# Optimization experiments

Measured on AMD Instinct MI355X. Metric: run time of the kernel, lower is better.

The kernel has to match this reference:

```python
import jax, jax.numpy as jnp
import numpy as np

B, K, D, DICT, C = 2048, 32, 768, 24576, 64


def setup_inputs() -> dict:
    key = jax.random.key(0)
    ks = jax.random.split(key, 9)
    up_vals = jax.random.uniform(ks[0], (B, K), dtype=jnp.float32)
    up_decoder_w = jax.random.normal(ks[1], (D, DICT), dtype=jnp.float32) * 0.02
    down_encoder_w = jax.random.normal(ks[2], (DICT, D), dtype=jnp.float32) * 0.02
    up_encoder_w = jax.random.normal(ks[3], (DICT, D), dtype=jnp.float32) * 0.02
    b_dec = jax.random.normal(ks[4], (D,), dtype=jnp.float32) * 0.02
    up_indices = jax.random.randint(ks[5], (B, K), 0, DICT)
    down_indices = jax.random.randint(ks[6], (B, K), 0, DICT)
    conn = jax.random.randint(ks[7], (DICT, C), 0, DICT)
    drop = jax.random.uniform(ks[8], (DICT, C)) < 0.1
    connections = jnp.where(drop, -1, conn)
    return {
        "up_vals": up_vals,
        "up_decoder_w": up_decoder_w,
        "down_encoder_w": down_encoder_w,
        "up_encoder_w": up_encoder_w,
        "b_dec": b_dec,
        "up_indices": up_indices,
        "down_indices": down_indices,
        "connections": connections,
    }


def reference(up_vals, up_decoder_w, down_encoder_w, up_encoder_w, b_dec,
              up_indices, down_indices, connections):
    # allowed upstream features per active downstream feature: [B, k_down, C]
    allowed = connections[down_indices]
    valid = allowed != -1
    # match[b,i,c,j] = allowed[b,i,c] == up_indices[b,j] (and slot valid)
    match = (allowed[..., None] == up_indices[:, None, None, :]) & valid[..., None]
    # multiplicity of each (down i, up j) pair across the C slots: [B, k_down, k_up]
    mult = match.sum(axis=2).astype(up_vals.dtype)
    # gather active decoder/encoder vectors
    act_up = up_decoder_w.T[up_indices]          # [B, k_up, D]
    act_down = down_encoder_w[down_indices]      # [B, k_down, D]
    # virtual weights between active down and up features
    vw = jnp.einsum('bid,bjd->bij', act_down, act_up)  # [B, k_down, k_up]
    contributions = jnp.einsum('bij,bij->bi', vw, mult * up_vals[:, None, :])
    # bias contribution (note: indexed by up_indices, broadcast add as in source)
    b_dec_contrib = up_encoder_w @ b_dec         # [DICT]
    return contributions + b_dec_contrib[up_indices]
```

## Files before the change

kernel.cpp:

```cpp
#include <hip/hip_runtime.h>

#define B_    2048
#define K_    32
#define D_    768
#define DICT_ 24576
#define C_    64

#define PAIR_CAP (1 << 18)
#define CCHUNK   512
#define DCHUNK   16
#define NCC      (DICT_ / CCHUNK)
#define NDC      (D_ / DCHUNK)

#define BDC_F (PAIR_CAP * 4)
#define CNT_F (BDC_F + DICT_)
#define T_F   (CNT_F + 1)
#define WS_FLOATS (T_F + PAIR_CAP)

__global__ void bdc_kernel(const float* __restrict__ up_enc,
                           const float* __restrict__ b_dec,
                           float* __restrict__ bdc,
                           int* __restrict__ cnt) {
    if (blockIdx.x == 0 && threadIdx.x == 0) cnt[0] = 0;
    int wave = threadIdx.x >> 6;
    int lane = threadIdx.x & 63;
    int row  = blockIdx.x * 4 + wave;
    const float4* rp = (const float4*)(up_enc + (size_t)row * D_);
    const float4* bp = (const float4*)b_dec;
    float acc = 0.f;
    #pragma unroll
    for (int i = 0; i < 3; ++i) {
        float4 a = rp[lane + 64 * i];
        float4 b = bp[lane + 64 * i];
        acc += a.x * b.x + a.y * b.y + a.z * b.z + a.w * b.w;
    }
    #pragma unroll
    for (int off = 32; off; off >>= 1) acc += __shfl_xor(acc, off);
    if (lane == 0) bdc[row] = acc;
}

__global__ void scan_kernel(const float* __restrict__ up_vals,
                            const float* __restrict__ bdc,
                            const int*   __restrict__ up_idx,
                            const int*   __restrict__ down_idx,
                            const int*   __restrict__ conn,
                            int*  __restrict__ cnt,
                            int*  __restrict__ tArr,
                            int4* __restrict__ recArr,
                            float* __restrict__ out) {
    int wave = threadIdx.x >> 6;
    int lane = threadIdx.x & 63;
    int item = blockIdx.x * 4 + wave;
    int b    = item >> 5;

    int di = down_idx[item];
    int allowed = conn[(size_t)di * C_ + lane];
    bool valid = allowed >= 0;
    int   myup  = up_idx[b * K_ + (lane & 31)];
    float myval = up_vals[b * K_ + (lane & 31)];

    if (lane == 0) out[item] = bdc[up_idx[item]];

    unsigned jm = 0u;
    #pragma unroll
    for (int j = 0; j < K_; ++j) {
        int tgt = __builtin_amdgcn_readlane(myup, j);
        jm |= (valid && (allowed == tgt)) ? (1u << j) : 0u;
    }

    if (__ballot(jm != 0u)) {
        #pragma unroll 1
        for (int j = 0; j < K_; ++j) {
            unsigned long long m = __ballot((jm >> j) & 1u);
            if (m != 0) {
                int   t = __shfl(myup, j);
                float w = (float)__popcll(m) * __shfl(myval, j);
                if (lane == 0) {
                    int pos = atomicAdd(cnt, 1);
                    if (pos < PAIR_CAP) {
                        tArr[pos]   = t;
                        recArr[pos] = make_int4(item, di, __float_as_int(w), 0);
                    }
                }
            }
        }
    }
}

__global__ __launch_bounds__(256) void pair_dot_kernel(const float* __restrict__ A,
                                                       const float* __restrict__ down_enc,
                                                       const int*  __restrict__ cnt,
                                                       const int*  __restrict__ tArr,
                                                       const int4* __restrict__ recArr,
                                                       float* __restrict__ out) {
    __shared__ float tile[DCHUNK * CCHUNK];
    __shared__ int   lidx[512];
    __shared__ int   lcnt;
    int tid = threadIdx.x;
    if (tid == 0) lcnt = 0;
    __syncthreads();

    int cc = blockIdx.x, dc = blockIdx.y;
    int c0 = cc * CCHUNK, d0 = dc * DCHUNK;

    int n = *cnt; if (n > PAIR_CAP) n = PAIR_CAP;
    for (int i = tid; i < n; i += 256) {
        if ((tArr[i] >> 9) == cc) {
            int s = atomicAdd(&lcnt, 1);
            if (s < 512) lidx[s] = i;
        }
    }
    __syncthreads();
    int ln = lcnt < 512 ? lcnt : 512;
    if (ln == 0) return;

    #pragma unroll
    for (int k = 0; k < 8; ++k) {
        int l  = tid + 256 * k;
        int r  = l >> 7, fi = l & 127;
        ((float4*)tile)[l] = *(const float4*)(A + (size_t)(d0 + r) * DICT_ + c0 + 4 * fi);
    }
    __syncthreads();

    for (int i = tid; i < ln; i += 256) {
        int idx = lidx[i];
        int4 rec = recArr[idx];
        int t = tArr[idx] - c0;
        const float4* dp = (const float4*)(down_enc + (size_t)rec.y * D_ + d0);
        float acc = 0.f;
        #pragma unroll
        for (int q = 0; q < 4; ++q) {
            float4 dv = dp[q];
            acc += dv.x * tile[(4 * q + 0) * CCHUNK + t]
                 + dv.y * tile[(4 * q + 1) * CCHUNK + t]
                 + dv.z * tile[(4 * q + 2) * CCHUNK + t]
                 + dv.w * tile[(4 * q + 3) * CCHUNK + t];
        }
        atomicAdd(out + rec.x, __int_as_float(rec.z) * acc);
    }
}

__global__ void main_fallback(const float* __restrict__ up_vals,
                              const float* __restrict__ up_dec,
                              const float* __restrict__ down_enc,
                              const float* __restrict__ up_enc,
                              const float* __restrict__ b_dec,
                              const int*   __restrict__ up_idx,
                              const int*   __restrict__ down_idx,
                              const int*   __restrict__ conn,
                              float* __restrict__ out) {
    int wave = threadIdx.x >> 6;
    int lane = threadIdx.x & 63;
    int item = blockIdx.x * 4 + wave;
    int b    = item >> 5;

    int di = down_idx[item];
    int allowed = conn[(size_t)di * C_ + lane];
    bool valid = allowed >= 0;
    int   myup  = up_idx[b * K_ + (lane & 31)];
    float myval = up_vals[b * K_ + (lane & 31)];

    unsigned jm = 0u;
    #pragma unroll
    for (int j = 0; j < K_; ++j) {
        int tgt = __builtin_amdgcn_readlane(myup, j);
        jm |= (valid && (allowed == tgt)) ? (1u << j) : 0u;
    }

    float acc = 0.f;
    if (__ballot(jm != 0u)) {
        const float* drow = down_enc + (size_t)di * D_;
        #pragma unroll 1
        for (int j = 0; j < K_; ++j) {
            unsigned long long m = __ballot((jm >> j) & 1u);
            if (m != 0) {
                float w   = (float)__popcll(m) * __shfl(myval, j);
                int   tgt = __shfl(myup, j);
                const float* colp = up_dec + tgt;
                float partial = 0.f;
                #pragma unroll
                for (int ii = 0; ii < 12; ++ii) {
                    int d = lane + 64 * ii;
                    partial += drow[d] * colp[(size_t)d * DICT_];
                }
                acc += w * partial;
            }
        }
    }

    {
        int ui = up_idx[item];
        const float4* rp = (const float4*)(up_enc + (size_t)ui * D_);
        const float4* bp = (const float4*)b_dec;
        #pragma unroll
        for (int ii = 0; ii < 3; ++ii) {
            float4 a  = rp[lane + 64 * ii];
            float4 bb = bp[lane + 64 * ii];
            acc += a.x * bb.x + a.y * bb.y + a.z * bb.z + a.w * bb.w;
        }
    }

    #pragma unroll
    for (int off = 32; off; off >>= 1) acc += __shfl_xor(acc, off);
    if (lane == 0) out[item] = acc;
}

extern "C" void kernel_launch(void* const* d_in, const int* in_sizes, int n_in,
                              void* d_out, int out_size, void* d_ws, size_t ws_size,
                              hipStream_t stream) {
    (void)in_sizes; (void)n_in; (void)out_size;
    const float* up_vals  = (const float*)d_in[0];
    const float* up_dec   = (const float*)d_in[1];
    const float* down_enc = (const float*)d_in[2];
    const float* up_enc   = (const float*)d_in[3];
    const float* b_dec    = (const float*)d_in[4];
    const int*   up_idx   = (const int*)d_in[5];
    const int*   down_idx = (const int*)d_in[6];
    const int*   conn     = (const int*)d_in[7];
    float* out = (float*)d_out;

    if (ws_size < (size_t)WS_FLOATS * sizeof(float)) {
        main_fallback<<<(B_ * K_) / 4, 256, 0, stream>>>(up_vals, up_dec, down_enc,
                                                         up_enc, b_dec, up_idx,
                                                         down_idx, conn, out);
        return;
    }

    float* ws     = (float*)d_ws;
    int4*  recArr = (int4*)ws;
    float* bdc    = ws + BDC_F;
    int*   cnt    = (int*)(ws + CNT_F);
    int*   tArr   = (int*)(ws + T_F);

    bdc_kernel<<<DICT_ / 4, 256, 0, stream>>>(up_enc, b_dec, bdc, cnt);
    scan_kernel<<<(B_ * K_) / 4, 256, 0, stream>>>(up_vals, bdc, up_idx, down_idx,
                                                   conn, cnt, tArr, recArr, out);
    pair_dot_kernel<<<dim3(NCC, NDC), 256, 0, stream>>>(up_dec, down_enc, cnt,
                                                        tArr, recArr, out);
}
```

Baseline: 293.6 us.

## Bucket matched pairs by dictionary chunk during scan instead of filtering later

The scan kernel now appends each matched (item, down, weight, up) record straight into a per-chunk bucket, using a separate padded atomic counter per chunk. Before, it wrote to one global list, and every pair_dot block rescanned that whole list to pick out its own entries. Bucketing removes that redundant full-list scan across all 48x48 blocks and drops the shared-memory index list. The trade-off is one atomic per bucket. A fixed cap of 2048 per bucket could silently drop pairs if a chunk overflows, though the expected pair count here is small.

```diff
diff --git a/kernel.cpp b/kernel.cpp
--- a/kernel.cpp
+++ b/kernel.cpp
@@ -6,22 +6,22 @@
 #define DICT_ 24576
 #define C_    64
 
-#define PAIR_CAP (1 << 18)
 #define CCHUNK   512
 #define DCHUNK   16
 #define NCC      (DICT_ / CCHUNK)
 #define NDC      (D_ / DCHUNK)
-
-#define BDC_F (PAIR_CAP * 4)
+#define BCAP     2048
+
+#define REC_F 0
+#define BDC_F (NCC * BCAP * 4)
 #define CNT_F (BDC_F + DICT_)
-#define T_F   (CNT_F + 1)
-#define WS_FLOATS (T_F + PAIR_CAP)
+#define WS_FLOATS (CNT_F + NCC * 16)
 
 __global__ void bdc_kernel(const float* __restrict__ up_enc,
                            const float* __restrict__ b_dec,
                            float* __restrict__ bdc,
                            int* __restrict__ cnt) {
-    if (blockIdx.x == 0 && threadIdx.x == 0) cnt[0] = 0;
+    if (blockIdx.x == 0 && threadIdx.x < NCC) cnt[threadIdx.x * 16] = 0;
     int wave = threadIdx.x >> 6;
     int lane = threadIdx.x & 63;
     int row  = blockIdx.x * 4 + wave;
@@ -45,8 +45,7 @@
                             const int*   __restrict__ down_idx,
                             const int*   __restrict__ conn,
                             int*  __restrict__ cnt,
-                            int*  __restrict__ tArr,
-                            int4* __restrict__ recArr,
+                            int4* __restrict__ recs,
                             float* __restrict__ out) {
     int wave = threadIdx.x >> 6;
     int lane = threadIdx.x & 63;
@@ -76,11 +75,10 @@
                 int   t = __shfl(myup, j);
                 float w = (float)__popcll(m) * __shfl(myval, j);
                 if (lane == 0) {
-                    int pos = atomicAdd(cnt, 1);
-                    if (pos < PAIR_CAP) {
-                        tArr[pos]   = t;
-                        recArr[pos] = make_int4(item, di, __float_as_int(w), 0);
-                    }
+                    int bi  = t >> 9;
+                    int pos = atomicAdd(cnt + bi * 16, 1);
+                    if (pos < BCAP)
+                        recs[bi * BCAP + pos] = make_int4(item, di, __float_as_int(w), t);
                 }
             }
         }
@@ -90,29 +88,16 @@
 __global__ __launch_bounds__(256) void pair_dot_kernel(const float* __restrict__ A,
                                                        const float* __restrict__ down_enc,
                                                        const int*  __restrict__ cnt,
-                                                       const int*  __restrict__ tArr,
-                                                       const int4* __restrict__ recArr,
+                                                       const int4* __restrict__ recs,
                                                        float* __restrict__ out) {
     __shared__ float tile[DCHUNK * CCHUNK];
-    __shared__ int   lidx[512];
-    __shared__ int   lcnt;
     int tid = threadIdx.x;
-    if (tid == 0) lcnt = 0;
-    __syncthreads();
-
     int cc = blockIdx.x, dc = blockIdx.y;
     int c0 = cc * CCHUNK, d0 = dc * DCHUNK;
 
-    int n = *cnt; if (n > PAIR_CAP) n = PAIR_CAP;
-    for (int i = tid; i < n; i += 256) {
-        if ((tArr[i] >> 9) == cc) {
-            int s = atomicAdd(&lcnt, 1);
-            if (s < 512) lidx[s] = i;
-        }
-    }
-    __syncthreads();
-    int ln = lcnt < 512 ? lcnt : 512;
-    if (ln == 0) return;
+    int n = cnt[cc * 16];
+    if (n > BCAP) n = BCAP;
+    if (n == 0) return;
 
     #pragma unroll
     for (int k = 0; k < 8; ++k) {
@@ -122,10 +107,10 @@
     }
     __syncthreads();
 
-    for (int i = tid; i < ln; i += 256) {
-        int idx = lidx[i];
-        int4 rec = recArr[idx];
-        int t = tArr[idx] - c0;
+    const int4* bucket = recs + (size_t)cc * BCAP;
+    for (int i = tid; i < n; i += 256) {
+        int4 rec = bucket[i];
+        int t = rec.w - c0;
         const float4* dp = (const float4*)(down_enc + (size_t)rec.y * D_ + d0);
         float acc = 0.f;
         #pragma unroll
@@ -226,15 +211,14 @@
         return;
     }
 
-    float* ws     = (float*)d_ws;
-    int4*  recArr = (int4*)ws;
-    float* bdc    = ws + BDC_F;
-    int*   cnt    = (int*)(ws + CNT_F);
-    int*   tArr   = (int*)(ws + T_F);
+    float* ws   = (float*)d_ws;
+    int4*  recs = (int4*)(ws + REC_F);
+    float* bdc  = ws + BDC_F;
+    int*   cnt  = (int*)(ws + CNT_F);
 
     bdc_kernel<<<DICT_ / 4, 256, 0, stream>>>(up_enc, b_dec, bdc, cnt);
     scan_kernel<<<(B_ * K_) / 4, 256, 0, stream>>>(up_vals, bdc, up_idx, down_idx,
-                                                   conn, cnt, tArr, recArr, out);
+                                                   conn, cnt, recs, out);
     pair_dot_kernel<<<dim3(NCC, NDC), 256, 0, stream>>>(up_dec, down_enc, cnt,
-                                                        tArr, recArr, out);
-}
+                                                        recs, out);
+}
```

Result: faster. 240.6 us (-18.0%).
